# Kernel optimization log

Hardware: AMD Instinct MI355X
Metric: run time of the kernel (lower is better)

## Reference

```python
import jax, jax.numpy as jnp
import numpy as np

B, S, D_IN, D_OUT = 4, 2048, 1024, 1024

def setup_inputs() -> dict:
    key = jax.random.key(0)
    k1, k2, k3, k4 = jax.random.split(key, 4)
    s = 0.02
    return {
        "X": jax.random.normal(k1, (B, S, D_IN), dtype=jnp.float32),
        "Wq": jax.random.normal(k2, (D_OUT, D_IN), dtype=jnp.float32) * s,
        "Wk": jax.random.normal(k3, (D_OUT, D_IN), dtype=jnp.float32) * s,
        "Wv": jax.random.normal(k4, (D_OUT, D_IN), dtype=jnp.float32) * s,
    }

def reference(X, Wq, Wk, Wv):
    # nn.Linear: y = x @ W.T (no bias)
    q = jnp.einsum('bsd,ed->bse', X, Wq)  # [B,S,D_OUT]
    k = jnp.einsum('bsd,ed->bse', X, Wk)
    v = jnp.einsum('bsd,ed->bse', X, Wv)
    scores = jnp.einsum('bqe,bke->bqk', q, k)  # [B,S,S]
    n = X.shape[1]
    causal = jnp.triu(jnp.ones((n, n), dtype=bool), k=1)
    scores = jnp.where(causal[None], -jnp.inf, scores)
    scale = 1.0 / jnp.sqrt(jnp.asarray(k.shape[-1], dtype=scores.dtype))
    attn = jax.nn.softmax(scores * scale, axis=-1)
    return jnp.einsum('bqk,bke->bqe', attn, v)
```

## Files before the change

kernel.cpp:

```cpp
#include <hip/hip_runtime.h>
#include <cstdint>


typedef __attribute__((ext_vector_type(8))) __bf16 bf16x8;
typedef __attribute__((ext_vector_type(4))) float f32x4;

#define BK 64

__device__ __forceinline__ unsigned short f2bf(float f) {
  union { float f; unsigned u; } v; v.f = f;
  unsigned r = v.u + 0x7fffu + ((v.u >> 16) & 1u);
  return (unsigned short)(r >> 16);
}

__device__ __forceinline__ void gload_lds16(const void* g, void* l) {
  __builtin_amdgcn_global_load_lds(
      (const __attribute__((address_space(1))) void*)g,
      (__attribute__((address_space(3))) void*)l, 16, 0, 0);
}

__global__ __launch_bounds__(256)
void cvt_all(const float* __restrict__ X, const float* __restrict__ Wq,
             const float* __restrict__ Wk, const float* __restrict__ Wv,
             unsigned short* __restrict__ Xbf, unsigned short* __restrict__ Wall) {
  const int bid = blockIdx.x;
  const float* src;
  unsigned short* dst;
  int i;
  if (bid < 8192) {
    src = X; dst = Xbf; i = bid * 256 + threadIdx.x;
  } else {
    const int m = bid - 8192;
    const int sel = m >> 10;
    src = (sel == 0) ? Wq : (sel == 1) ? Wk : Wv;
    dst = Wall + (size_t)sel * 1048576;
    i = (m & 1023) * 256 + threadIdx.x;
  }
  float4 v = ((const float4*)src)[i];
  ushort4 o;
  o.x = f2bf(v.x); o.y = f2bf(v.y); o.z = f2bf(v.z); o.w = f2bf(v.w);
  ((ushort4*)dst)[i] = o;
}

__global__ __launch_bounds__(256)
void gemm_qkv(const unsigned short* __restrict__ A,
              const unsigned short* __restrict__ Bm,
              unsigned short* __restrict__ Qb,
              unsigned short* __restrict__ Kb,
              unsigned short* __restrict__ Vt)
{
  const int bx = blockIdx.x, by = blockIdx.y;

  __shared__ __align__(16) unsigned short As[128 * BK];
  __shared__ __align__(16) unsigned short Bs[128 * BK];

  const int tid = threadIdx.x;
  const int wave = tid >> 6, lane = tid & 63;
  const int wr = wave >> 1, wc = wave & 1;
  const int quad = lane >> 4, l16 = lane & 15;

  const int rsub = wave * 8 + (lane >> 3);
  const int csw = ((lane & 7) ^ ((lane >> 3) & 7)) * 8;

  const unsigned short* aS[4];
  const unsigned short* bS[4];
  #pragma unroll
  for (int s = 0; s < 4; ++s) {
    aS[s] = A + (size_t)(by * 128 + s * 32 + rsub) * 1024 + csw;
    bS[s] = Bm + (size_t)(bx * 128 + s * 32 + rsub) * 1024 + csw;
  }

  f32x4 acc[4][4];
  #pragma unroll
  for (int i = 0; i < 4; ++i)
    #pragma unroll
    for (int j = 0; j < 4; ++j)
      acc[i][j] = (f32x4){0.f, 0.f, 0.f, 0.f};

  const int pq = (quad ^ (l16 & 7)) * 8;
  const int aOff = (wr * 64 + l16) * BK + pq;
  const int bOff = (wc * 64 + l16) * BK + pq;

  for (int k0 = 0; k0 < 1024; k0 += BK) {
    #pragma unroll
    for (int s = 0; s < 4; ++s) {
      gload_lds16(aS[s] + k0, As + s * 2048 + wave * 512);
      gload_lds16(bS[s] + k0, Bs + s * 2048 + wave * 512);
    }
    __syncthreads();
    #pragma unroll
    for (int h = 0; h < 2; ++h) {
      const int hx = h * 32;
      bf16x8 af[4], bfr[4];
      #pragma unroll
      for (int i = 0; i < 4; ++i)
        af[i] = *(const bf16x8*)(As + ((aOff + i * 16 * BK) ^ hx));
      #pragma unroll
      for (int j = 0; j < 4; ++j)
        bfr[j] = *(const bf16x8*)(Bs + ((bOff + j * 16 * BK) ^ hx));
      #pragma unroll
      for (int i = 0; i < 4; ++i)
        #pragma unroll
        for (int j = 0; j < 4; ++j)
          acc[i][j] = __builtin_amdgcn_mfma_f32_16x16x32_bf16(af[i], bfr[j], acc[i][j], 0, 0, 0);
    }
    __syncthreads();
  }

  const int row0 = by * 128 + wr * 64 + quad * 4;
  const int col0 = bx * 128 + wc * 64 + l16;
  if (bx < 16) {
    unsigned short* C = (bx < 8) ? Qb : Kb;
    const int col = (bx < 8) ? col0 : col0 - 1024;
    #pragma unroll
    for (int i = 0; i < 4; ++i)
      #pragma unroll
      for (int r = 0; r < 4; ++r) {
        const size_t rr = (size_t)(row0 + i * 16 + r) * 1024;
        #pragma unroll
        for (int j = 0; j < 4; ++j)
          C[rr + col + j * 16] = f2bf(acc[i][j][r]);
      }
  } else {
    const int b = row0 >> 11;
    const int s0 = row0 & 2047;
    unsigned short* Vb = Vt + (size_t)b * 2097152;
    #pragma unroll
    for (int j = 0; j < 4; ++j) {
      const size_t ee = (size_t)(col0 - 2048 + j * 16) * 2048;
      #pragma unroll
      for (int i = 0; i < 4; ++i) {
        ushort4 o;
        o.x = f2bf(acc[i][j][0]); o.y = f2bf(acc[i][j][1]);
        o.z = f2bf(acc[i][j][2]); o.w = f2bf(acc[i][j][3]);
        *(ushort4*)(Vb + ee + s0 + i * 16) = o;
      }
    }
  }
}

__global__ __launch_bounds__(256)
void gemm_scores(const unsigned short* __restrict__ Q,
                 const unsigned short* __restrict__ Km,
                 unsigned short* __restrict__ S,
                 float* __restrict__ L)
{
  const int t = blockIdx.x;
  const int bz = blockIdx.z;
  int by = (int)((sqrtf(8.f * t + 1.f) - 1.f) * 0.5f);
  while ((by + 1) * (by + 2) / 2 <= t) ++by;
  while (by * (by + 1) / 2 > t) --by;
  const int bx = t - by * (by + 1) / 2;

  __shared__ __align__(16) unsigned short As[128 * BK];
  __shared__ __align__(16) unsigned short Bs[128 * BK];

  const unsigned short* Ab = Q + (size_t)bz * 2097152;
  const unsigned short* Bb = Km + (size_t)bz * 2097152;

  const int tid = threadIdx.x;
  const int wave = tid >> 6, lane = tid & 63;
  const int wr = wave >> 1, wc = wave & 1;
  const int quad = lane >> 4, l16 = lane & 15;

  const int rsub = wave * 8 + (lane >> 3);
  const int csw = ((lane & 7) ^ ((lane >> 3) & 7)) * 8;

  const unsigned short* aS[4];
  const unsigned short* bS[4];
  #pragma unroll
  for (int s = 0; s < 4; ++s) {
    aS[s] = Ab + (size_t)(by * 128 + s * 32 + rsub) * 1024 + csw;
    bS[s] = Bb + (size_t)(bx * 128 + s * 32 + rsub) * 1024 + csw;
  }

  f32x4 acc[4][4];
  #pragma unroll
  for (int i = 0; i < 4; ++i)
    #pragma unroll
    for (int j = 0; j < 4; ++j)
      acc[i][j] = (f32x4){0.f, 0.f, 0.f, 0.f};

  const int pq = (quad ^ (l16 & 7)) * 8;
  const int aOff = (wr * 64 + l16) * BK + pq;
  const int bOff = (wc * 64 + l16) * BK + pq;

  for (int k0 = 0; k0 < 1024; k0 += BK) {
    #pragma unroll
    for (int s = 0; s < 4; ++s) {
      gload_lds16(aS[s] + k0, As + s * 2048 + wave * 512);
      gload_lds16(bS[s] + k0, Bs + s * 2048 + wave * 512);
    }
    __syncthreads();
    #pragma unroll
    for (int h = 0; h < 2; ++h) {
      const int hx = h * 32;
      bf16x8 af[4], bfr[4];
      #pragma unroll
      for (int i = 0; i < 4; ++i)
        af[i] = *(const bf16x8*)(As + ((aOff + i * 16 * BK) ^ hx));
      #pragma unroll
      for (int j = 0; j < 4; ++j)
        bfr[j] = *(const bf16x8*)(Bs + ((bOff + j * 16 * BK) ^ hx));
      #pragma unroll
      for (int i = 0; i < 4; ++i)
        #pragma unroll
        for (int j = 0; j < 4; ++j)
          acc[i][j] = __builtin_amdgcn_mfma_f32_16x16x32_bf16(af[i], bfr[j], acc[i][j], 0, 0, 0);
    }
    __syncthreads();
  }

  const int row0 = by * 128 + wr * 64 + quad * 4;
  const int col0 = bx * 128 + wc * 64 + l16;
  float* Lb = L + (size_t)bz * 2048;
  unsigned short* C = S + (size_t)bz * 4194304;

  #pragma unroll
  for (int i = 0; i < 4; ++i)
    #pragma unroll
    for (int r = 0; r < 4; ++r) {
      const int grow = row0 + i * 16 + r;
      float ps = 0.f;
      #pragma unroll
      for (int j = 0; j < 4; ++j) {
        const int gcol = col0 + j * 16;
        float e = (gcol <= grow) ? __expf(acc[i][j][r] * 0.03125f) : 0.f;
        acc[i][j][r] = e;
        ps += e;
      }
      #pragma unroll
      for (int m = 8; m > 0; m >>= 1)
        ps += __shfl_xor(ps, m);
      if (l16 == 0) atomicAdd(&Lb[grow], ps);
      const size_t rr = (size_t)grow * 2048;
      #pragma unroll
      for (int j = 0; j < 4; ++j)
        C[rr + col0 + j * 16] = f2bf(acc[i][j][r]);
    }
}

__global__ __launch_bounds__(256)
void gemm_pv(const unsigned short* __restrict__ P,
             const unsigned short* __restrict__ Vt,
             float* __restrict__ Out,
             const float* __restrict__ L)
{
  const int bx = blockIdx.x, by = blockIdx.y, bz = blockIdx.z;

  __shared__ __align__(16) unsigned short As[128 * BK];
  __shared__ __align__(16) unsigned short Bs[128 * BK];

  const unsigned short* Ab = P + (size_t)bz * 4194304;
  const unsigned short* Bb = Vt + (size_t)bz * 2097152;

  const int tid = threadIdx.x;
  const int wave = tid >> 6, lane = tid & 63;
  const int wr = wave >> 1, wc = wave & 1;
  const int quad = lane >> 4, l16 = lane & 15;

  const int rsub = wave * 8 + (lane >> 3);
  const int csw = ((lane & 7) ^ ((lane >> 3) & 7)) * 8;

  const unsigned short* aS[4];
  const unsigned short* bS[4];
  #pragma unroll
  for (int s = 0; s < 4; ++s) {
    aS[s] = Ab + (size_t)(by * 128 + s * 32 + rsub) * 2048 + csw;
    bS[s] = Bb + (size_t)(bx * 128 + s * 32 + rsub) * 2048 + csw;
  }

  f32x4 acc[4][4];
  #pragma unroll
  for (int i = 0; i < 4; ++i)
    #pragma unroll
    for (int j = 0; j < 4; ++j)
      acc[i][j] = (f32x4){0.f, 0.f, 0.f, 0.f};

  const int kmax = (by + 1) * 128;

  const int pq = (quad ^ (l16 & 7)) * 8;
  const int aOff = (wr * 64 + l16) * BK + pq;
  const int bOff = (wc * 64 + l16) * BK + pq;

  for (int k0 = 0; k0 < kmax; k0 += BK) {
    #pragma unroll
    for (int s = 0; s < 4; ++s) {
      gload_lds16(aS[s] + k0, As + s * 2048 + wave * 512);
      gload_lds16(bS[s] + k0, Bs + s * 2048 + wave * 512);
    }
    __syncthreads();
    #pragma unroll
    for (int h = 0; h < 2; ++h) {
      const int hx = h * 32;
      bf16x8 af[4], bfr[4];
      #pragma unroll
      for (int i = 0; i < 4; ++i)
        af[i] = *(const bf16x8*)(As + ((aOff + i * 16 * BK) ^ hx));
      #pragma unroll
      for (int j = 0; j < 4; ++j)
        bfr[j] = *(const bf16x8*)(Bs + ((bOff + j * 16 * BK) ^ hx));
      #pragma unroll
      for (int i = 0; i < 4; ++i)
        #pragma unroll
        for (int j = 0; j < 4; ++j)
          acc[i][j] = __builtin_amdgcn_mfma_f32_16x16x32_bf16(af[i], bfr[j], acc[i][j], 0, 0, 0);
    }
    __syncthreads();
  }

  const int row0 = by * 128 + wr * 64 + quad * 4;
  const int col0 = bx * 128 + wc * 64 + l16;
  float* C = Out + (size_t)bz * 2097152;
  const float* Lb = L + (size_t)bz * 2048;
  #pragma unroll
  for (int i = 0; i < 4; ++i)
    #pragma unroll
    for (int r = 0; r < 4; ++r) {
      const int grow = row0 + i * 16 + r;
      const float inv = 1.0f / Lb[grow];
      const size_t rr = (size_t)grow * 1024;
      #pragma unroll
      for (int j = 0; j < 4; ++j)
        C[rr + col0 + j * 16] = acc[i][j][r] * inv;
    }
}

extern "C" void kernel_launch(void* const* d_in, const int* in_sizes, int n_in,
                              void* d_out, int out_size, void* d_ws, size_t ws_size,
                              hipStream_t stream) {
  const float* X  = (const float*)d_in[0];
  const float* Wq = (const float*)d_in[1];
  const float* Wk = (const float*)d_in[2];
  const float* Wv = (const float*)d_in[3];
  float* Out = (float*)d_out;

  char* ws = (char*)d_ws;
  unsigned short* Xbf  = (unsigned short*)(ws);
  unsigned short* Wall = (unsigned short*)(ws + 16777216);
  unsigned short* Qbf  = (unsigned short*)(ws + 23068672);
  unsigned short* Kbf  = (unsigned short*)(ws + 39845888);
  unsigned short* Vt   = (unsigned short*)(ws + 56623104);
  unsigned short* Sbf  = (unsigned short*)(ws + 73400320);
  float*          Lbuf = (float*)(ws);

  cvt_all<<<11264, 256, 0, stream>>>(X, Wq, Wk, Wv, Xbf, Wall);

  gemm_qkv<<<dim3(24, 64), 256, 0, stream>>>(Xbf, Wall, Qbf, Kbf, Vt);

  hipMemsetAsync(Lbuf, 0, 4 * 2048 * sizeof(float), stream);

  gemm_scores<<<dim3(136, 1, 4), 256, 0, stream>>>(Qbf, Kbf, Sbf, Lbuf);

  gemm_pv<<<dim3(8, 16, 4), 256, 0, stream>>>(Sbf, Vt, Out, Lbuf);
}
```

Measured before the change: 245.7 us.

## Fold L zeroing into convert kernel, use 32-bit load offsets, add occupancy hints

Removes the separate memset launch by having four extra blocks of the conversion kernel zero the row-sum buffer, which now sits in its own workspace region. The three GEMM kernels compute global-to-LDS load addresses as 32-bit byte offsets from a base pointer instead of 64-bit per-slice pointers, cutting address arithmetic and register use. They also gain a min-blocks-per-CU launch bound of 3, which may force register spills. The aim is less launch overhead and more resident waves, with the risk that the tighter register budget hurts the MFMA loop.

```diff
diff --git a/kernel.cpp b/kernel.cpp
--- a/kernel.cpp
+++ b/kernel.cpp
@@ -22,8 +22,15 @@
 __global__ __launch_bounds__(256)
 void cvt_all(const float* __restrict__ X, const float* __restrict__ Wq,
              const float* __restrict__ Wk, const float* __restrict__ Wv,
-             unsigned short* __restrict__ Xbf, unsigned short* __restrict__ Wall) {
+             unsigned short* __restrict__ Xbf, unsigned short* __restrict__ Wall,
+             float* __restrict__ L) {
   const int bid = blockIdx.x;
+  if (bid >= 11264) {
+    float4* p = (float4*)(L + (size_t)(bid - 11264) * 2048);
+    p[threadIdx.x] = (float4){0.f, 0.f, 0.f, 0.f};
+    p[threadIdx.x + 256] = (float4){0.f, 0.f, 0.f, 0.f};
+    return;
+  }
   const float* src;
   unsigned short* dst;
   int i;
@@ -42,7 +49,7 @@
   ((ushort4*)dst)[i] = o;
 }
 
-__global__ __launch_bounds__(256)
+__global__ __launch_bounds__(256, 3)
 void gemm_qkv(const unsigned short* __restrict__ A,
               const unsigned short* __restrict__ Bm,
               unsigned short* __restrict__ Qb,
@@ -59,16 +66,17 @@
   const int wr = wave >> 1, wc = wave & 1;
   const int quad = lane >> 4, l16 = lane & 15;
 
-  const int rsub = wave * 8 + (lane >> 3);
-  const int csw = ((lane & 7) ^ ((lane >> 3) & 7)) * 8;
-
-  const unsigned short* aS[4];
-  const unsigned short* bS[4];
+  const unsigned rsub = wave * 8 + (lane >> 3);
+  const unsigned csb = (unsigned)(((lane & 7) ^ ((lane >> 3) & 7)) * 16);
+
+  unsigned offA[4], offB[4];
   #pragma unroll
   for (int s = 0; s < 4; ++s) {
-    aS[s] = A + (size_t)(by * 128 + s * 32 + rsub) * 1024 + csw;
-    bS[s] = Bm + (size_t)(bx * 128 + s * 32 + rsub) * 1024 + csw;
-  }
+    offA[s] = ((unsigned)(by * 128 + s * 32 + rsub) * 1024u) * 2u + csb;
+    offB[s] = ((unsigned)(bx * 128 + s * 32 + rsub) * 1024u) * 2u + csb;
+  }
+  const char* Abase = (const char*)A;
+  const char* Bbase = (const char*)Bm;
 
   f32x4 acc[4][4];
   #pragma unroll
@@ -82,10 +90,11 @@
   const int bOff = (wc * 64 + l16) * BK + pq;
 
   for (int k0 = 0; k0 < 1024; k0 += BK) {
+    const unsigned kb = (unsigned)k0 * 2u;
     #pragma unroll
     for (int s = 0; s < 4; ++s) {
-      gload_lds16(aS[s] + k0, As + s * 2048 + wave * 512);
-      gload_lds16(bS[s] + k0, Bs + s * 2048 + wave * 512);
+      gload_lds16(Abase + kb + offA[s], As + s * 2048 + wave * 512);
+      gload_lds16(Bbase + kb + offB[s], Bs + s * 2048 + wave * 512);
     }
     __syncthreads();
     #pragma unroll
@@ -139,7 +148,7 @@
   }
 }
 
-__global__ __launch_bounds__(256)
+__global__ __launch_bounds__(256, 3)
 void gemm_scores(const unsigned short* __restrict__ Q,
                  const unsigned short* __restrict__ Km,
                  unsigned short* __restrict__ S,
@@ -155,24 +164,22 @@
   __shared__ __align__(16) unsigned short As[128 * BK];
   __shared__ __align__(16) unsigned short Bs[128 * BK];
 
-  const unsigned short* Ab = Q + (size_t)bz * 2097152;
-  const unsigned short* Bb = Km + (size_t)bz * 2097152;
-
   const int tid = threadIdx.x;
   const int wave = tid >> 6, lane = tid & 63;
   const int wr = wave >> 1, wc = wave & 1;
   const int quad = lane >> 4, l16 = lane & 15;
 
-  const int rsub = wave * 8 + (lane >> 3);
-  const int csw = ((lane & 7) ^ ((lane >> 3) & 7)) * 8;
-
-  const unsigned short* aS[4];
-  const unsigned short* bS[4];
+  const unsigned rsub = wave * 8 + (lane >> 3);
+  const unsigned csb = (unsigned)(((lane & 7) ^ ((lane >> 3) & 7)) * 16);
+
+  unsigned offA[4], offB[4];
   #pragma unroll
   for (int s = 0; s < 4; ++s) {
-    aS[s] = Ab + (size_t)(by * 128 + s * 32 + rsub) * 1024 + csw;
-    bS[s] = Bb + (size_t)(bx * 128 + s * 32 + rsub) * 1024 + csw;
-  }
+    offA[s] = ((unsigned)(by * 128 + s * 32 + rsub) * 1024u) * 2u + csb;
+    offB[s] = ((unsigned)(bx * 128 + s * 32 + rsub) * 1024u) * 2u + csb;
+  }
+  const char* Abase = (const char*)(Q + (size_t)bz * 2097152);
+  const char* Bbase = (const char*)(Km + (size_t)bz * 2097152);
 
   f32x4 acc[4][4];
   #pragma unroll
@@ -186,10 +193,11 @@
   const int bOff = (wc * 64 + l16) * BK + pq;
 
   for (int k0 = 0; k0 < 1024; k0 += BK) {
+    const unsigned kb = (unsigned)k0 * 2u;
     #pragma unroll
     for (int s = 0; s < 4; ++s) {
-      gload_lds16(aS[s] + k0, As + s * 2048 + wave * 512);
-      gload_lds16(bS[s] + k0, Bs + s * 2048 + wave * 512);
+      gload_lds16(Abase + kb + offA[s], As + s * 2048 + wave * 512);
+      gload_lds16(Bbase + kb + offB[s], Bs + s * 2048 + wave * 512);
     }
     __syncthreads();
     #pragma unroll
@@ -240,7 +248,7 @@
     }
 }
 
-__global__ __launch_bounds__(256)
+__global__ __launch_bounds__(256, 3)
 void gemm_pv(const unsigned short* __restrict__ P,
              const unsigned short* __restrict__ Vt,
              float* __restrict__ Out,
@@ -251,24 +259,22 @@
   __shared__ __align__(16) unsigned short As[128 * BK];
   __shared__ __align__(16) unsigned short Bs[128 * BK];
 
-  const unsigned short* Ab = P + (size_t)bz * 4194304;
-  const unsigned short* Bb = Vt + (size_t)bz * 2097152;
-
   const int tid = threadIdx.x;
   const int wave = tid >> 6, lane = tid & 63;
   const int wr = wave >> 1, wc = wave & 1;
   const int quad = lane >> 4, l16 = lane & 15;
 
-  const int rsub = wave * 8 + (lane >> 3);
-  const int csw = ((lane & 7) ^ ((lane >> 3) & 7)) * 8;
-
-  const unsigned short* aS[4];
-  const unsigned short* bS[4];
+  const unsigned rsub = wave * 8 + (lane >> 3);
+  const unsigned csb = (unsigned)(((lane & 7) ^ ((lane >> 3) & 7)) * 16);
+
+  unsigned offA[4], offB[4];
   #pragma unroll
   for (int s = 0; s < 4; ++s) {
-    aS[s] = Ab + (size_t)(by * 128 + s * 32 + rsub) * 2048 + csw;
-    bS[s] = Bb + (size_t)(bx * 128 + s * 32 + rsub) * 2048 + csw;
-  }
+    offA[s] = ((unsigned)(by * 128 + s * 32 + rsub) * 2048u) * 2u + csb;
+    offB[s] = ((unsigned)(bx * 128 + s * 32 + rsub) * 2048u) * 2u + csb;
+  }
+  const char* Abase = (const char*)(P + (size_t)bz * 4194304);
+  const char* Bbase = (const char*)(Vt + (size_t)bz * 2097152);
 
   f32x4 acc[4][4];
   #pragma unroll
@@ -284,10 +290,11 @@
   const int bOff = (wc * 64 + l16) * BK + pq;
 
   for (int k0 = 0; k0 < kmax; k0 += BK) {
+    const unsigned kb = (unsigned)k0 * 2u;
     #pragma unroll
     for (int s = 0; s < 4; ++s) {
-      gload_lds16(aS[s] + k0, As + s * 2048 + wave * 512);
-      gload_lds16(bS[s] + k0, Bs + s * 2048 + wave * 512);
+      gload_lds16(Abase + kb + offA[s], As + s * 2048 + wave * 512);
+      gload_lds16(Bbase + kb + offB[s], Bs + s * 2048 + wave * 512);
     }
     __syncthreads();
     #pragma unroll
@@ -342,14 +349,12 @@
   unsigned short* Kbf  = (unsigned short*)(ws + 39845888);
   unsigned short* Vt   = (unsigned short*)(ws + 56623104);
   unsigned short* Sbf  = (unsigned short*)(ws + 73400320);
-  float*          Lbuf = (float*)(ws);
-
-  cvt_all<<<11264, 256, 0, stream>>>(X, Wq, Wk, Wv, Xbf, Wall);
+  float*          Lbuf = (float*)(ws + 106954752);
+
+  cvt_all<<<11268, 256, 0, stream>>>(X, Wq, Wk, Wv, Xbf, Wall, Lbuf);
 
   gemm_qkv<<<dim3(24, 64), 256, 0, stream>>>(Xbf, Wall, Qbf, Kbf, Vt);
 
-  hipMemsetAsync(Lbuf, 0, 4 * 2048 * sizeof(float), stream);
-
   gemm_scores<<<dim3(136, 1, 4), 256, 0, stream>>>(Qbf, Kbf, Sbf, Lbuf);
 
   gemm_pv<<<dim3(8, 16, 4), 256, 0, stream>>>(Sbf, Vt, Out, Lbuf);
```

After: 228.4 us. -7.0%, faster.
